# Performance work log

Hardware: AMD Instinct MI355X
Metric: run time of the kernel (lower is better)

The kernel has to match this reference:

```python
import jax, jax.numpy as jnp
import numpy as np

SPARSITY = 0.9   # config.pruning_parameters.sparsity (self.r)
TEMP = 0.01      # config.pruning_parameters.temperature
D_MODEL, D_FF = 4096, 16384


def setup_inputs() -> dict:
    key = jax.random.key(0)
    weight = jax.random.normal(key, (D_MODEL, D_FF), dtype=jnp.float32)
    return {"weight": weight}


def reference(weight):
    # PDP.get_mask (unstructured path) followed by mask * weight.
    n = weight.size  # static
    # Full descending sort of |weight|, exactly as ops.top_k(abs_flat, size)
    w_all = jax.lax.top_k(jnp.abs(weight).ravel(), n)[0]
    # ind = cast((1 - r) * N, int32) - 1, clipped to [0, N-2]; static since shapes are static
    ind = int((1.0 - SPARSITY) * n) - 1
    lim = min(max(ind, 0), n - 2)
    Wh = w_all[lim]
    Wt = w_all[lim + 1]
    t = 0.5 * (Wh + Wt)  # threshold order statistic
    # softmax over the pair (t^2, w^2)/temp, keep second component:
    # mw = exp(w^2/T) / (exp(t^2/T) + exp(w^2/T)) = sigmoid((w^2 - t^2)/T)
    mw = jax.nn.sigmoid((weight * weight - t * t) / TEMP)
    return mw * weight
```

## Files before the change

kernel.cpp:

```cpp
#include <hip/hip_runtime.h>
#include <hip/hip_bf16.h>


#define NBC 4096
#define NBF 12288

typedef float  v4f  __attribute__((ext_vector_type(4)));
typedef unsigned v4u __attribute__((ext_vector_type(4)));

__global__ void zero_ws(unsigned* __restrict__ ws, int n) {
    int i = blockIdx.x * blockDim.x + threadIdx.x;
    if (i < n) ws[i] = 0;
}

__global__ void sample_hist(const v4u* __restrict__ in, unsigned* __restrict__ gh) {
    __shared__ unsigned h[NBC];
    for (int i = threadIdx.x; i < NBC; i += blockDim.x) h[i] = 0;
    __syncthreads();
    const v4u* p = in + (size_t)blockIdx.x * 16384;
    #pragma unroll
    for (int k = 0; k < 4; ++k) {
        v4u v = p[threadIdx.x + k * 256];
        atomicAdd(&h[(v.x & 0x7fffffffu) >> 19], 1u);
        atomicAdd(&h[(v.y & 0x7fffffffu) >> 19], 1u);
        atomicAdd(&h[(v.z & 0x7fffffffu) >> 19], 1u);
        atomicAdd(&h[(v.w & 0x7fffffffu) >> 19], 1u);
    }
    __syncthreads();
    for (int i = threadIdx.x; i < NBC; i += blockDim.x) {
        unsigned c = h[i];
        if (c) atomicAdd(&gh[i], c);
    }
}

__global__ void scan_sample(const unsigned* __restrict__ gh, unsigned* __restrict__ res,
                            unsigned sample_need) {
    __shared__ unsigned bins[NBC];
    __shared__ unsigned part[256];
    __shared__ unsigned sup[16];
    unsigned s = 0;
    for (int j = 0; j < 16; ++j) {
        int idx = threadIdx.x * 16 + j;
        unsigned c = gh[NBC - 1 - idx];
        bins[idx] = c;
        s += c;
    }
    part[threadIdx.x] = s;
    __syncthreads();
    if (threadIdx.x < 16) {
        unsigned t = 0;
        for (int j = 0; j < 16; ++j) t += part[threadIdx.x * 16 + j];
        sup[threadIdx.x] = t;
    }
    __syncthreads();
    if (threadIdx.x == 0) {
        unsigned accum = 0; int sb = 15;
        for (int i = 0; i < 16; ++i) { unsigned nx = accum + sup[i]; if (nx >= sample_need) { sb = i; break; } accum = nx; }
        int pb = sb * 16 + 15;
        for (int i = sb * 16; i < sb * 16 + 16; ++i) { unsigned nx = accum + part[i]; if (nx >= sample_need) { pb = i; break; } accum = nx; }
        int d = pb * 16 + 15;
        for (int i = pb * 16; i < pb * 16 + 16; ++i) { unsigned nx = accum + bins[i]; if (nx >= sample_need) { d = i; break; } accum = nx; }
        unsigned b_est = (unsigned)(NBC - 1 - d);
        res[0] = (b_est > 0) ? b_est - 1u : 0u;
        res[1] = (b_est < NBC - 1) ? b_est + 1u : (unsigned)(NBC - 1);
    }
}

__global__ void fine_hist(const v4u* __restrict__ in, unsigned* __restrict__ res,
                          unsigned* __restrict__ gh, int n4) {
    __shared__ unsigned h[NBF];
    __shared__ unsigned red[256];
    const unsigned lo = res[0] << 19;
    const unsigned hi = (res[1] + 1u) << 19;
    for (int i = threadIdx.x; i < NBF; i += blockDim.x) h[i] = 0;
    __syncthreads();
    unsigned above = 0;
    int stride = gridDim.x * blockDim.x;
    for (int i = blockIdx.x * blockDim.x + threadIdx.x; i < n4; i += stride) {
        v4u v = in[i];
        #pragma unroll
        for (int k = 0; k < 4; ++k) {
            unsigned u = v[k] & 0x7fffffffu;
            if (u >= hi) ++above;
            else if (u >= lo) atomicAdd(&h[(u - lo) >> 7], 1u);
        }
    }
    red[threadIdx.x] = above;
    __syncthreads();
    for (int s = 128; s > 0; s >>= 1) {
        if (threadIdx.x < (unsigned)s) red[threadIdx.x] += red[threadIdx.x + s];
        __syncthreads();
    }
    if (threadIdx.x == 0 && red[0]) atomicAdd(&res[2], red[0]);
    for (int i = threadIdx.x; i < NBF; i += blockDim.x) {
        unsigned c = h[i];
        if (c) atomicAdd(&gh[i], c);
    }
}

__global__ void scan_fine(const unsigned* __restrict__ gh, unsigned* __restrict__ res,
                          unsigned need_h, unsigned need_t) {
    __shared__ unsigned bins[NBF];
    __shared__ unsigned part[256];
    __shared__ unsigned sup[16];
    unsigned s = 0;
    for (int j = 0; j < 48; ++j) {
        int idx = threadIdx.x * 48 + j;
        unsigned c = gh[NBF - 1 - idx];
        bins[idx] = c;
        s += c;
    }
    part[threadIdx.x] = s;
    __syncthreads();
    if (threadIdx.x < 16) {
        unsigned t = 0;
        for (int j = 0; j < 16; ++j) t += part[threadIdx.x * 16 + j];
        sup[threadIdx.x] = t;
    }
    __syncthreads();
    if (threadIdx.x == 0) {
        const unsigned lo = res[0] << 19;
        const unsigned base = res[2];
        unsigned keyh = 0, keyt = 0;
        {
            unsigned accum = base; int sb = 15;
            for (int i = 0; i < 16; ++i) { unsigned nx = accum + sup[i]; if (nx >= need_h) { sb = i; break; } accum = nx; }
            int pb = sb * 16 + 15;
            for (int i = sb * 16; i < sb * 16 + 16; ++i) { unsigned nx = accum + part[i]; if (nx >= need_h) { pb = i; break; } accum = nx; }
            int d = NBF - 1;
            for (int i = pb * 48; i < pb * 48 + 48; ++i) { unsigned nx = accum + bins[i]; if (nx >= need_h) { d = i; break; } accum = nx; }
            keyh = (unsigned)(NBF - 1 - d);
        }
        {
            unsigned accum = base; int sb = 15;
            for (int i = 0; i < 16; ++i) { unsigned nx = accum + sup[i]; if (nx >= need_t) { sb = i; break; } accum = nx; }
            int pb = sb * 16 + 15;
            for (int i = sb * 16; i < sb * 16 + 16; ++i) { unsigned nx = accum + part[i]; if (nx >= need_t) { pb = i; break; } accum = nx; }
            int d = NBF - 1;
            for (int i = pb * 48; i < pb * 48 + 48; ++i) { unsigned nx = accum + bins[i]; if (nx >= need_t) { d = i; break; } accum = nx; }
            keyt = (unsigned)(NBF - 1 - d);
        }
        float Wh = __uint_as_float(lo + (keyh << 7) + 64u);
        float Wt = __uint_as_float(lo + (keyt << 7) + 64u);
        float t  = 0.5f * (Wh + Wt);
        res[3] = __float_as_uint(t * t);
    }
}

__global__ void apply_mask(const v4f* __restrict__ in, v4f* __restrict__ out,
                           const unsigned* __restrict__ res, int n4) {
    float t2 = __uint_as_float(res[3]);
    int stride = gridDim.x * blockDim.x;
    for (int i = blockIdx.x * blockDim.x + threadIdx.x; i < n4; i += stride) {
        v4f w = __builtin_nontemporal_load(&in[i]);
        v4f o;
        o.x = w.x * __builtin_amdgcn_rcpf(1.0f + __expf((t2 - w.x * w.x) * 100.0f));
        o.y = w.y * __builtin_amdgcn_rcpf(1.0f + __expf((t2 - w.y * w.y) * 100.0f));
        o.z = w.z * __builtin_amdgcn_rcpf(1.0f + __expf((t2 - w.z * w.z) * 100.0f));
        o.w = w.w * __builtin_amdgcn_rcpf(1.0f + __expf((t2 - w.w * w.w) * 100.0f));
        __builtin_nontemporal_store(o, &out[i]);
    }
}

extern "C" void kernel_launch(void* const* d_in, const int* in_sizes, int n_in,
                              void* d_out, int out_size, void* d_ws, size_t ws_size,
                              hipStream_t stream) {
    const int n = in_sizes[0];
    const int n4 = n / 4;
    const v4u* in4 = (const v4u*)d_in[0];

    unsigned* ws     = (unsigned*)d_ws;
    unsigned* hist_s = ws;
    unsigned* hist_f = ws + NBC;
    unsigned* res    = ws + NBC + NBF;

    int ind = (int)((1.0 - 0.9) * (double)n) - 1;
    int lim = ind < 0 ? 0 : ind;
    if (lim > n - 2) lim = n - 2;
    unsigned need_h = (unsigned)lim + 1u;
    unsigned need_t = (unsigned)lim + 2u;

    const unsigned SAMPLE = 1024u * 4096u;
    unsigned sample_need = (unsigned)((double)need_h * (double)SAMPLE / (double)n);
    if (sample_need == 0) sample_need = 1;

    zero_ws<<<(NBC + NBF + 8 + 255) / 256, 256, 0, stream>>>(ws, NBC + NBF + 8);
    sample_hist<<<1024, 256, 0, stream>>>(in4, hist_s);
    scan_sample<<<1, 256, 0, stream>>>(hist_s, res, sample_need);
    fine_hist<<<4096, 256, 0, stream>>>(in4, res, hist_f, n4);
    scan_fine<<<1, 256, 0, stream>>>(hist_f, res, need_h, need_t);
    apply_mask<<<8192, 256, 0, stream>>>((const v4f*)d_in[0], (v4f*)d_out, res, n4);
}
```

Measured before the change: 558.6 us.

## Add second sampled refinement pass to shrink fine histogram to 2048 bins

Inserts a sampled fine-histogram pass over the first 1024×16384 vectors, which narrows the threshold window to 2048 bins of width 128 ulps. The full-data fine_hist can then use a much smaller shared histogram (2048 instead of 12288 entries), so zeroing and flushing per block cost less, and its loop is unrolled by two loads. It also switches apply_mask from nontemporal loads to normal loads. The risk is correctness: if the sample-based window misses the true order statistic, the result is wrong, and the extra pass adds two kernel launches plus a read of part of the input.

```diff
diff --git a/kernel.cpp b/kernel.cpp
--- a/kernel.cpp
+++ b/kernel.cpp
@@ -1,11 +1,11 @@
 #include <hip/hip_runtime.h>
-#include <hip/hip_bf16.h>
-
-
-#define NBC 4096
-#define NBF 12288
-
-typedef float  v4f  __attribute__((ext_vector_type(4)));
+
+
+#define NBC  4096
+#define NBSF 12288
+#define NBF2 2048
+
+typedef float    v4f __attribute__((ext_vector_type(4)));
 typedef unsigned v4u __attribute__((ext_vector_type(4)));
 
 __global__ void zero_ws(unsigned* __restrict__ ws, int n) {
@@ -66,21 +66,22 @@
     }
 }
 
-__global__ void fine_hist(const v4u* __restrict__ in, unsigned* __restrict__ res,
-                          unsigned* __restrict__ gh, int n4) {
-    __shared__ unsigned h[NBF];
+__global__ void sample_fine_hist(const v4u* __restrict__ in, unsigned* __restrict__ res,
+                                 unsigned* __restrict__ gh) {
+    __shared__ unsigned h[NBSF];
     __shared__ unsigned red[256];
     const unsigned lo = res[0] << 19;
     const unsigned hi = (res[1] + 1u) << 19;
-    for (int i = threadIdx.x; i < NBF; i += blockDim.x) h[i] = 0;
+    for (int i = threadIdx.x; i < NBSF; i += blockDim.x) h[i] = 0;
     __syncthreads();
     unsigned above = 0;
-    int stride = gridDim.x * blockDim.x;
-    for (int i = blockIdx.x * blockDim.x + threadIdx.x; i < n4; i += stride) {
-        v4u v = in[i];
-        #pragma unroll
-        for (int k = 0; k < 4; ++k) {
-            unsigned u = v[k] & 0x7fffffffu;
+    const v4u* p = in + (size_t)blockIdx.x * 16384;
+    #pragma unroll
+    for (int k = 0; k < 4; ++k) {
+        v4u v = p[threadIdx.x + k * 256];
+        #pragma unroll
+        for (int j = 0; j < 4; ++j) {
+            unsigned u = v[j] & 0x7fffffffu;
             if (u >= hi) ++above;
             else if (u >= lo) atomicAdd(&h[(u - lo) >> 7], 1u);
         }
@@ -91,22 +92,22 @@
         if (threadIdx.x < (unsigned)s) red[threadIdx.x] += red[threadIdx.x + s];
         __syncthreads();
     }
-    if (threadIdx.x == 0 && red[0]) atomicAdd(&res[2], red[0]);
-    for (int i = threadIdx.x; i < NBF; i += blockDim.x) {
+    if (threadIdx.x == 0 && red[0]) atomicAdd(&res[4], red[0]);
+    for (int i = threadIdx.x; i < NBSF; i += blockDim.x) {
         unsigned c = h[i];
         if (c) atomicAdd(&gh[i], c);
     }
 }
 
-__global__ void scan_fine(const unsigned* __restrict__ gh, unsigned* __restrict__ res,
-                          unsigned need_h, unsigned need_t) {
-    __shared__ unsigned bins[NBF];
+__global__ void scan_sample2(const unsigned* __restrict__ gh, unsigned* __restrict__ res,
+                             unsigned sample_need) {
+    __shared__ unsigned bins[NBSF];
     __shared__ unsigned part[256];
     __shared__ unsigned sup[16];
     unsigned s = 0;
     for (int j = 0; j < 48; ++j) {
         int idx = threadIdx.x * 48 + j;
-        unsigned c = gh[NBF - 1 - idx];
+        unsigned c = gh[NBSF - 1 - idx];
         bins[idx] = c;
         s += c;
     }
@@ -119,29 +120,107 @@
     }
     __syncthreads();
     if (threadIdx.x == 0) {
-        const unsigned lo = res[0] << 19;
+        unsigned accum = res[4];
+        int sb = 15;
+        for (int i = 0; i < 16; ++i) { unsigned nx = accum + sup[i]; if (nx >= sample_need) { sb = i; break; } accum = nx; }
+        int pb = sb * 16 + 15;
+        for (int i = sb * 16; i < sb * 16 + 16; ++i) { unsigned nx = accum + part[i]; if (nx >= sample_need) { pb = i; break; } accum = nx; }
+        int d = pb * 48 + 47;
+        for (int i = pb * 48; i < pb * 48 + 48; ++i) { unsigned nx = accum + bins[i]; if (nx >= sample_need) { d = i; break; } accum = nx; }
+        int kc = NBSF - 1 - d;
+        int kb = kc - (NBF2 / 2);
+        if (kb < 0) kb = 0;
+        if (kb > NBSF - NBF2) kb = NBSF - NBF2;
+        res[5] = (unsigned)kb;
+    }
+}
+
+__global__ void fine_hist(const v4u* __restrict__ in, unsigned* __restrict__ res,
+                          unsigned* __restrict__ gh, int n4) {
+    __shared__ unsigned h[NBF2];
+    __shared__ unsigned red[256];
+    const unsigned lo2 = (res[0] << 19) + (res[5] << 7);
+    const unsigned hi2 = lo2 + ((unsigned)NBF2 << 7);
+    for (int i = threadIdx.x; i < NBF2; i += blockDim.x) h[i] = 0;
+    __syncthreads();
+    unsigned above = 0;
+    const int stride = gridDim.x * blockDim.x;
+    int i = blockIdx.x * blockDim.x + threadIdx.x;
+    for (; i + stride < n4; i += 2 * stride) {
+        v4u a = in[i];
+        v4u b = in[i + stride];
+        #pragma unroll
+        for (int k = 0; k < 4; ++k) {
+            unsigned u = a[k] & 0x7fffffffu;
+            if (u >= hi2) ++above;
+            else if (u >= lo2) atomicAdd(&h[(u - lo2) >> 7], 1u);
+        }
+        #pragma unroll
+        for (int k = 0; k < 4; ++k) {
+            unsigned u = b[k] & 0x7fffffffu;
+            if (u >= hi2) ++above;
+            else if (u >= lo2) atomicAdd(&h[(u - lo2) >> 7], 1u);
+        }
+    }
+    if (i < n4) {
+        v4u a = in[i];
+        #pragma unroll
+        for (int k = 0; k < 4; ++k) {
+            unsigned u = a[k] & 0x7fffffffu;
+            if (u >= hi2) ++above;
+            else if (u >= lo2) atomicAdd(&h[(u - lo2) >> 7], 1u);
+        }
+    }
+    red[threadIdx.x] = above;
+    __syncthreads();
+    for (int s = 128; s > 0; s >>= 1) {
+        if (threadIdx.x < (unsigned)s) red[threadIdx.x] += red[threadIdx.x + s];
+        __syncthreads();
+    }
+    if (threadIdx.x == 0 && red[0]) atomicAdd(&res[2], red[0]);
+    for (int i2 = threadIdx.x; i2 < NBF2; i2 += blockDim.x) {
+        unsigned c = h[i2];
+        if (c) atomicAdd(&gh[i2], c);
+    }
+}
+
+__global__ void scan_fine(const unsigned* __restrict__ gh, unsigned* __restrict__ res,
+                          unsigned need_h, unsigned need_t) {
+    __shared__ unsigned bins[NBF2];
+    __shared__ unsigned part[256];
+    __shared__ unsigned sup[16];
+    unsigned s = 0;
+    #pragma unroll
+    for (int j = 0; j < 8; ++j) {
+        int idx = threadIdx.x * 8 + j;
+        unsigned c = gh[NBF2 - 1 - idx];
+        bins[idx] = c;
+        s += c;
+    }
+    part[threadIdx.x] = s;
+    __syncthreads();
+    if (threadIdx.x < 16) {
+        unsigned t = 0;
+        for (int j = 0; j < 16; ++j) t += part[threadIdx.x * 16 + j];
+        sup[threadIdx.x] = t;
+    }
+    __syncthreads();
+    if (threadIdx.x == 0) {
+        const unsigned lo2 = (res[0] << 19) + (res[5] << 7);
         const unsigned base = res[2];
-        unsigned keyh = 0, keyt = 0;
-        {
+        unsigned needs[2] = { need_h, need_t };
+        unsigned keys[2];
+        for (int q = 0; q < 2; ++q) {
             unsigned accum = base; int sb = 15;
-            for (int i = 0; i < 16; ++i) { unsigned nx = accum + sup[i]; if (nx >= need_h) { sb = i; break; } accum = nx; }
+            for (int i = 0; i < 16; ++i) { unsigned nx = accum + sup[i]; if (nx >= needs[q]) { sb = i; break; } accum = nx; }
             int pb = sb * 16 + 15;
-            for (int i = sb * 16; i < sb * 16 + 16; ++i) { unsigned nx = accum + part[i]; if (nx >= need_h) { pb = i; break; } accum = nx; }
-            int d = NBF - 1;
-            for (int i = pb * 48; i < pb * 48 + 48; ++i) { unsigned nx = accum + bins[i]; if (nx >= need_h) { d = i; break; } accum = nx; }
-            keyh = (unsigned)(NBF - 1 - d);
-        }
-        {
-            unsigned accum = base; int sb = 15;
-            for (int i = 0; i < 16; ++i) { unsigned nx = accum + sup[i]; if (nx >= need_t) { sb = i; break; } accum = nx; }
-            int pb = sb * 16 + 15;
-            for (int i = sb * 16; i < sb * 16 + 16; ++i) { unsigned nx = accum + part[i]; if (nx >= need_t) { pb = i; break; } accum = nx; }
-            int d = NBF - 1;
-            for (int i = pb * 48; i < pb * 48 + 48; ++i) { unsigned nx = accum + bins[i]; if (nx >= need_t) { d = i; break; } accum = nx; }
-            keyt = (unsigned)(NBF - 1 - d);
-        }
-        float Wh = __uint_as_float(lo + (keyh << 7) + 64u);
-        float Wt = __uint_as_float(lo + (keyt << 7) + 64u);
+            for (int i = sb * 16; i < sb * 16 + 16; ++i) { unsigned nx = accum + part[i]; if (nx >= needs[q]) { pb = i; break; } accum = nx; }
+            int d = pb * 8 + 7;
+            for (int i = pb * 8; i < pb * 8 + 8; ++i) { unsigned nx = accum + bins[i]; if (nx >= needs[q]) { d = i; break; } accum = nx; }
+            keys[q] = (unsigned)(NBF2 - 1 - d);
+        }
+        float Wh = __uint_as_float(lo2 + (keys[0] << 7) + 64u);
+        float Wt = __uint_as_float(lo2 + (keys[1] << 7) + 64u);
         float t  = 0.5f * (Wh + Wt);
         res[3] = __float_as_uint(t * t);
     }
@@ -152,7 +231,7 @@
     float t2 = __uint_as_float(res[3]);
     int stride = gridDim.x * blockDim.x;
     for (int i = blockIdx.x * blockDim.x + threadIdx.x; i < n4; i += stride) {
-        v4f w = __builtin_nontemporal_load(&in[i]);
+        v4f w = in[i];
         v4f o;
         o.x = w.x * __builtin_amdgcn_rcpf(1.0f + __expf((t2 - w.x * w.x) * 100.0f));
         o.y = w.y * __builtin_amdgcn_rcpf(1.0f + __expf((t2 - w.y * w.y) * 100.0f));
@@ -169,10 +248,11 @@
     const int n4 = n / 4;
     const v4u* in4 = (const v4u*)d_in[0];
 
-    unsigned* ws     = (unsigned*)d_ws;
-    unsigned* hist_s = ws;
-    unsigned* hist_f = ws + NBC;
-    unsigned* res    = ws + NBC + NBF;
+    unsigned* ws      = (unsigned*)d_ws;
+    unsigned* hist_s  = ws;
+    unsigned* hist_sf = ws + NBC;
+    unsigned* hist_f  = ws + NBC + NBSF;
+    unsigned* res     = ws + NBC + NBSF + NBF2;
 
     int ind = (int)((1.0 - 0.9) * (double)n) - 1;
     int lim = ind < 0 ? 0 : ind;
@@ -184,9 +264,12 @@
     unsigned sample_need = (unsigned)((double)need_h * (double)SAMPLE / (double)n);
     if (sample_need == 0) sample_need = 1;
 
-    zero_ws<<<(NBC + NBF + 8 + 255) / 256, 256, 0, stream>>>(ws, NBC + NBF + 8);
+    const int nz = NBC + NBSF + NBF2 + 8;
+    zero_ws<<<(nz + 255) / 256, 256, 0, stream>>>(ws, nz);
     sample_hist<<<1024, 256, 0, stream>>>(in4, hist_s);
     scan_sample<<<1, 256, 0, stream>>>(hist_s, res, sample_need);
+    sample_fine_hist<<<1024, 256, 0, stream>>>(in4, res, hist_sf);
+    scan_sample2<<<1, 256, 0, stream>>>(hist_sf, res, sample_need);
     fine_hist<<<4096, 256, 0, stream>>>(in4, res, hist_f, n4);
     scan_fine<<<1, 256, 0, stream>>>(hist_f, res, need_h, need_t);
     apply_mask<<<8192, 256, 0, stream>>>((const v4f*)d_in[0], (v4f*)d_out, res, n4);
```

After: 544.7 us. 2.5% less time.
